# Kernel optimization log

Measured on AMD Instinct MI355X. Metric: run time of the kernel, lower is better.

## Reference

```python
import jax, jax.numpy as jnp
import numpy as np

POWERS = (0, 1, 2)
IN_F, OUT_F = 64, 64
B, N, T = 8, 2048, 12


def setup_inputs() -> dict:
    key = jax.random.key(0)
    ks = jax.random.split(key, 8)
    inp = {
        "x": jax.random.normal(ks[0], (B, IN_F, N, T), dtype=jnp.float32),
        "adj": jax.random.uniform(ks[1], (B, N, N), dtype=jnp.float32),
    }
    # Xavier-uniform weights per adjacency power, zero biases (as in initialize_weights)
    limit = float(np.sqrt(6.0 / (IN_F + OUT_F)))
    for i, p in enumerate(POWERS):
        inp[f"W{p}"] = jax.random.uniform(ks[2 + i], (IN_F, OUT_F), jnp.float32, -limit, limit)
        inp[f"b{p}"] = jnp.zeros((OUT_F,), jnp.float32)
    return inp


def _gcn_conv(x, adj, W, b, a_power):
    # x: [B, F, N, T]; W: [F, O]; adj: [B, N, N]
    h = jnp.einsum('bfnt,fo->bont', x, W) + b[None, :, None, None]
    # repeated diffusion along node axis: h[f, n] <- sum_m adj[n, m] h[f, m]
    for _ in range(a_power):
        h = jnp.einsum('bnm,bomt->bont', adj, h)
    return jax.nn.leaky_relu(h)  # default negative_slope 0.01, same as torch


def reference(x, adj, W0, b0, W1, b1, W2, b2):
    params = {0: (W0, b0), 1: (W1, b1), 2: (W2, b2)}
    outs = [_gcn_conv(x, adj, params[p][0], params[p][1], p) for p in POWERS]
    return jnp.concatenate(outs, axis=1)  # [B, len(POWERS)*O, N, T]
```

## Files before the change

### kernel.cpp

```cpp
#include <hip/hip_runtime.h>

#define B_ 8
#define N_ 2048
#define T_ 12
#define F_ 64
#define NT 24576
#define CH 192
#define C_ 768

typedef __bf16 bf16x8 __attribute__((ext_vector_type(8)));
typedef float f32x4 __attribute__((ext_vector_type(4)));

typedef const __attribute__((address_space(1))) unsigned int as1_uint;
typedef __attribute__((address_space(3))) unsigned int as3_uint;

__device__ __forceinline__ void gload16(const void* g, void* l) {
  __builtin_amdgcn_global_load_lds((as1_uint*)g, (as3_uint*)l, 16, 0, 0);
}

__device__ __forceinline__ unsigned short f2bf(float f) {
  unsigned int u = __float_as_uint(f);
  u += 0x7FFFu + ((u >> 16) & 1u);
  return (unsigned short)(u >> 16);
}

__device__ __forceinline__ float leaky(float v) {
  return v >= 0.0f ? v : 0.01f * v;
}

__global__ __launch_bounds__(256) void convert_adj_k(const float* __restrict__ adj,
                                                     unsigned short* __restrict__ adjb) {
  size_t i = (size_t)blockIdx.x * 256 + threadIdx.x;
  const float4 v = reinterpret_cast<const float4*>(adj)[i];
  ushort4 u;
  u.x = f2bf(v.x); u.y = f2bf(v.y); u.z = f2bf(v.z); u.w = f2bf(v.w);
  reinterpret_cast<ushort4*>(adjb)[i] = u;
}

__device__ __forceinline__ void stage_wt(const float* __restrict__ W,
                                         unsigned short* Wt, int tid) {
  const int f = tid >> 2;
  const int q = tid & 3;
  const float4* row = reinterpret_cast<const float4*>(W + f * 64 + q * 16);
#pragma unroll
  for (int v4 = 0; v4 < 4; ++v4) {
    float4 v = row[v4];
    const int ob = q * 16 + v4 * 4;
    Wt[(ob + 0) * 72 + f] = f2bf(v.x);
    Wt[(ob + 1) * 72 + f] = f2bf(v.y);
    Wt[(ob + 2) * 72 + f] = f2bf(v.z);
    Wt[(ob + 3) * 72 + f] = f2bf(v.w);
  }
}

__global__ __launch_bounds__(256) void p0_k(const float* __restrict__ x,
                                            const float* __restrict__ W0,
                                            const float* __restrict__ bia0,
                                            float* __restrict__ out) {
  __shared__ unsigned short Wt[64 * 72];
  __shared__ float bias[64];
  const int tid = threadIdx.x;
  stage_wt(W0, Wt, tid);
  if (tid < 64) bias[tid] = bia0[tid];
  __syncthreads();

  const int lane = tid & 63;
  const int wave = tid >> 6;
  const int b = blockIdx.y;
  const int e = blockIdx.x * 64 + wave * 16 + (lane & 15);
  const int fgrp = (lane >> 4) * 8;
  const float* xb = x + (size_t)b * F_ * NT;

  bf16x8 xf[2];
#pragma unroll
  for (int kf = 0; kf < 2; ++kf)
#pragma unroll
    for (int j = 0; j < 8; ++j)
      xf[kf][j] = (__bf16)xb[(size_t)(fgrp + kf * 32 + j) * NT + e];

  float* outb = out + (size_t)b * CH * NT;
#pragma unroll
  for (int ob = 0; ob < 4; ++ob) {
    f32x4 acc = {};
#pragma unroll
    for (int kf = 0; kf < 2; ++kf) {
      bf16x8 af = *reinterpret_cast<const bf16x8*>(
          &Wt[(ob * 16 + (lane & 15)) * 72 + kf * 32 + fgrp]);
      acc = __builtin_amdgcn_mfma_f32_16x16x32_bf16(af, xf[kf], acc, 0, 0, 0);
    }
#pragma unroll
    for (int r = 0; r < 4; ++r) {
      const int o = ob * 16 + (lane >> 4) * 4 + r;
      outb[(size_t)o * NT + e] = leaky(acc[r] + bias[o]);
    }
  }
}

__global__ __launch_bounds__(256) void p12_k(const float* __restrict__ x,
                                             const float* __restrict__ W1,
                                             const float* __restrict__ bia1,
                                             const float* __restrict__ W2,
                                             const float* __restrict__ bia2,
                                             unsigned short* __restrict__ G1,
                                             unsigned short* __restrict__ G2) {
  __shared__ unsigned short Wt[2][64 * 72];
  __shared__ float bias[2][64];
  const int tid = threadIdx.x;
  stage_wt(W1, Wt[0], tid);
  stage_wt(W2, Wt[1], tid);
  if (tid < 64) bias[0][tid] = bia1[tid];
  else if (tid < 128) bias[1][tid - 64] = bia2[tid - 64];
  __syncthreads();

  const int lane = tid & 63;
  const int wave = tid >> 6;
  const int b = blockIdx.y;
  const int n = blockIdx.x * 16 + (lane & 15);
  const int fgrp = (lane >> 4) * 8;
  const float* xb = x + (size_t)b * F_ * NT;
  unsigned short* Gp[2] = {G1 + (size_t)b * C_ * N_, G2 + (size_t)b * C_ * N_};

#pragma unroll
  for (int it = 0; it < 3; ++it) {
    const int t = wave * 3 + it;
    const int e = n * T_ + t;

    bf16x8 xf[2];
#pragma unroll
    for (int kf = 0; kf < 2; ++kf)
#pragma unroll
      for (int j = 0; j < 8; ++j)
        xf[kf][j] = (__bf16)xb[(size_t)(fgrp + kf * 32 + j) * NT + e];

#pragma unroll
    for (int p = 0; p < 2; ++p) {
#pragma unroll
      for (int ob = 0; ob < 4; ++ob) {
        f32x4 acc = {};
#pragma unroll
        for (int kf = 0; kf < 2; ++kf) {
          bf16x8 af = *reinterpret_cast<const bf16x8*>(
              &Wt[p][(ob * 16 + (lane & 15)) * 72 + kf * 32 + fgrp]);
          acc = __builtin_amdgcn_mfma_f32_16x16x32_bf16(af, xf[kf], acc, 0, 0, 0);
        }
#pragma unroll
        for (int r = 0; r < 4; ++r) {
          const int o = ob * 16 + (lane >> 4) * 4 + r;
          Gp[p][(size_t)(o * T_ + t) * N_ + n] = f2bf(acc[r] + bias[p][o]);
        }
      }
    }
  }
}

__global__ __launch_bounds__(512, 2) void gemm8_k(
    const unsigned short* __restrict__ adjb,
    const unsigned short* __restrict__ Bt,
    float* __restrict__ out,
    unsigned short* __restrict__ Ht,
    const int mode, const int ochan_base)
{
  extern __shared__ __align__(16) unsigned short lds[];

  const int tid  = threadIdx.x;
  const int lane = tid & 63;
  const int wave = tid >> 6;
  const int wr = wave >> 2;
  const int wc = wave & 3;

  const int b     = blockIdx.x & 7;
  const int w     = blockIdx.x >> 3;
  const int n0    = (w & 7) * 256;
  const int c0    = (w >> 3) * 256;

  const unsigned short* A  = adjb + (size_t)b * N_ * N_;
  const unsigned short* Bm = Bt   + (size_t)b * C_ * N_;

  const unsigned short* aSt = A  + (size_t)(n0 + wave * 32 + (lane >> 2)) * N_ + (lane & 3) * 8;
  const unsigned short* bSt = Bm + (size_t)(c0 + wave * 32 + (lane >> 2)) * N_ + (lane & 3) * 8;
  const int ldsStW = wave * 1024;

  const int aRd = (wr * 128 + (lane & 15)) * 32 + (lane >> 4) * 8;
  const int bRd = (wc * 64  + (lane & 15)) * 32 + (lane >> 4) * 8;

  f32x4 acc[8][4] = {};
  bf16x8 afr[4], bfr[4];

#define STG(BASEG, LDSB, KT, KH) \
  gload16((BASEG) + (KT) * 64 + (KH) * 32, lds + (LDSB) + (KH) * 8192 + ldsStW); \
  gload16((BASEG) + (size_t)16 * N_ + (KT) * 64 + (KH) * 32, \
          lds + (LDSB) + (KH) * 8192 + ldsStW + 512);

#define RD_B(BUFB, KH) { \
  _Pragma("unroll") \
  for (int nf = 0; nf < 4; ++nf) \
    bfr[nf] = *(const bf16x8*)(lds + (BUFB) + (KH) * 8192 + nf * 512 + bRd); }

#define RD_A(BUFA, KH, QM) { \
  _Pragma("unroll") \
  for (int mm = 0; mm < 4; ++mm) \
    afr[mm] = *(const bf16x8*)(lds + (BUFA) + (KH) * 8192 + (QM) * 2048 + mm * 512 + aRd); }

#define MFMA16(QM) { \
  _Pragma("unroll") \
  for (int mm = 0; mm < 4; ++mm) \
  _Pragma("unroll") \
  for (int nf = 0; nf < 4; ++nf) \
    acc[(QM) * 4 + mm][nf] = __builtin_amdgcn_mfma_f32_16x16x32_bf16( \
        afr[mm], bfr[nf], acc[(QM) * 4 + mm][nf], 0, 0, 0); }

#define MIDBAR() \
  __builtin_amdgcn_s_barrier(); \
  asm volatile("s_waitcnt lgkmcnt(0)" ::: "memory"); \
  __builtin_amdgcn_sched_barrier(0); \
  __builtin_amdgcn_s_setprio(1);

#define ENDBAR() \
  __builtin_amdgcn_s_setprio(0); \
  __builtin_amdgcn_s_barrier();

#define WAITV(N) asm volatile("s_waitcnt vmcnt(" #N ")" ::: "memory");

  STG(aSt, 0,     0, 0)  STG(bSt, 32768, 0, 0)
  STG(aSt, 0,     0, 1)  STG(bSt, 32768, 0, 1)
  STG(aSt, 16384, 1, 0)  STG(bSt, 49152, 1, 0)
  WAITV(8)
  __builtin_amdgcn_s_barrier();

#pragma unroll 1
  for (int it = 0; it < 15; ++it) {
    const int kt0 = 2 * it;
    RD_B(32768, 0) RD_A(0, 0, 0)
    STG(aSt, 16384, kt0 + 1, 1)
    MIDBAR() MFMA16(0) ENDBAR()
    RD_A(0, 0, 1)
    STG(bSt, 49152, kt0 + 1, 1)
    WAITV(8)
    MIDBAR() MFMA16(1) ENDBAR()
    RD_B(32768, 1) RD_A(0, 1, 0)
    STG(aSt, 0, kt0 + 2, 0)
    MIDBAR() MFMA16(0) ENDBAR()
    RD_A(0, 1, 1)
    STG(bSt, 32768, kt0 + 2, 0)
    WAITV(8)
    MIDBAR() MFMA16(1) ENDBAR()
    RD_B(49152, 0) RD_A(16384, 0, 0)
    STG(aSt, 0, kt0 + 2, 1)
    MIDBAR() MFMA16(0) ENDBAR()
    RD_A(16384, 0, 1)
    STG(bSt, 32768, kt0 + 2, 1)
    WAITV(8)
    MIDBAR() MFMA16(1) ENDBAR()
    RD_B(49152, 1) RD_A(16384, 1, 0)
    STG(aSt, 16384, kt0 + 3, 0)
    MIDBAR() MFMA16(0) ENDBAR()
    RD_A(16384, 1, 1)
    STG(bSt, 49152, kt0 + 3, 0)
    WAITV(8)
    MIDBAR() MFMA16(1) ENDBAR()
  }

  {
    RD_B(32768, 0) RD_A(0, 0, 0)
    STG(aSt, 16384, 31, 1)
    MIDBAR() MFMA16(0) ENDBAR()
    RD_A(0, 0, 1)
    STG(bSt, 49152, 31, 1)
    WAITV(8)
    MIDBAR() MFMA16(1) ENDBAR()
    RD_B(32768, 1) RD_A(0, 1, 0)
    MIDBAR() MFMA16(0) ENDBAR()
    RD_A(0, 1, 1)
    WAITV(4)
    MIDBAR() MFMA16(1) ENDBAR()
    RD_B(49152, 0) RD_A(16384, 0, 0)
    MIDBAR() MFMA16(0) ENDBAR()
    RD_A(16384, 0, 1)
    WAITV(0)
    MIDBAR() MFMA16(1) ENDBAR()
    RD_B(49152, 1) RD_A(16384, 1, 0)
    MIDBAR() MFMA16(0) ENDBAR()
    RD_A(16384, 1, 1)
    MIDBAR() MFMA16(1) ENDBAR()
  }

  const int r4 = (lane >> 4) * 4;
  if (mode == 0) {
    float* outb = out + (size_t)b * CH * NT;
#pragma unroll
    for (int m = 0; m < 8; ++m) {
#pragma unroll
      for (int nf = 0; nf < 4; ++nf) {
        const int c = c0 + wc * 64 + nf * 16 + (lane & 15);
        const int o = c / 12;
        const int t = c - o * 12;
#pragma unroll
        for (int r = 0; r < 4; ++r) {
          const int n = n0 + wr * 128 + m * 16 + r4 + r;
          outb[((size_t)(ochan_base + o) * N_ + n) * T_ + t] = leaky(acc[m][nf][r]);
        }
      }
    }
  } else {
    unsigned short* Hb = Ht + (size_t)b * C_ * N_;
#pragma unroll
    for (int m = 0; m < 8; ++m) {
#pragma unroll
      for (int nf = 0; nf < 4; ++nf) {
        const int c = c0 + wc * 64 + nf * 16 + (lane & 15);
        const int nb = n0 + wr * 128 + m * 16 + r4;
        ushort4 u;
        u.x = f2bf(acc[m][nf][0]);
        u.y = f2bf(acc[m][nf][1]);
        u.z = f2bf(acc[m][nf][2]);
        u.w = f2bf(acc[m][nf][3]);
        *reinterpret_cast<ushort4*>(&Hb[(size_t)c * N_ + nb]) = u;
      }
    }
  }
#undef STG
#undef RD_B
#undef RD_A
#undef MFMA16
#undef MIDBAR
#undef ENDBAR
#undef WAITV
}

extern "C" void kernel_launch(void* const* d_in, const int* in_sizes, int n_in,
                              void* d_out, int out_size, void* d_ws, size_t ws_size,
                              hipStream_t stream) {
  const float* x   = (const float*)d_in[0];
  const float* adj = (const float*)d_in[1];
  const float* W0  = (const float*)d_in[2];
  const float* b0  = (const float*)d_in[3];
  const float* W1  = (const float*)d_in[4];
  const float* b1  = (const float*)d_in[5];
  const float* W2  = (const float*)d_in[6];
  const float* b2  = (const float*)d_in[7];
  float* out = (float*)d_out;

  char* ws = (char*)d_ws;
  unsigned short* adjb = (unsigned short*)ws;
  unsigned short* G1   = (unsigned short*)(ws + 67108864);
  unsigned short* G2   = (unsigned short*)(ws + 92274688);
  unsigned short* Ht   = G1;

  hipFuncSetAttribute((const void*)gemm8_k,
                      hipFuncAttributeMaxDynamicSharedMemorySize, 131072);

  hipLaunchKernelGGL(convert_adj_k, dim3((B_ * N_ * N_ / 4) / 256), dim3(256), 0, stream,
                     adj, adjb);

  hipLaunchKernelGGL(p0_k, dim3(NT / 64, B_), dim3(256), 0, stream,
                     x, W0, b0, out);

  hipLaunchKernelGGL(p12_k, dim3(N_ / 16, B_), dim3(256), 0, stream,
                     x, W1, b1, W2, b2, G1, G2);

  hipLaunchKernelGGL(gemm8_k, dim3(192), dim3(512), 131072, stream,
                     adjb, G1, out, (unsigned short*)nullptr, 0, 64);

  hipLaunchKernelGGL(gemm8_k, dim3(192), dim3(512), 131072, stream,
                     adjb, G2, out, Ht, 1, 0);

  hipLaunchKernelGGL(gemm8_k, dim3(192), dim3(512), 131072, stream,
                     adjb, Ht, out, (unsigned short*)nullptr, 0, 128);
}
```

Measured before the change: 293.4 us.

## Shrink GEMM column tile to 192 for 256 blocks and swizzle LDS layout

```diff
diff --git a/kernel.cpp b/kernel.cpp
--- a/kernel.cpp
+++ b/kernel.cpp
@@ -168,32 +168,36 @@
   const int wr = wave >> 2;
   const int wc = wave & 3;
 
-  const int b     = blockIdx.x & 7;
-  const int w     = blockIdx.x >> 3;
-  const int n0    = (w & 7) * 256;
-  const int c0    = (w >> 3) * 256;
+  const int b  = blockIdx.x & 7;
+  const int w  = blockIdx.x >> 3;
+  const int n0 = (w & 7) * 256;
+  const int c0 = (w >> 3) * 192;
 
   const unsigned short* A  = adjb + (size_t)b * N_ * N_;
   const unsigned short* Bm = Bt   + (size_t)b * C_ * N_;
 
-  const unsigned short* aSt = A  + (size_t)(n0 + wave * 32 + (lane >> 2)) * N_ + (lane & 3) * 8;
-  const unsigned short* bSt = Bm + (size_t)(c0 + wave * 32 + (lane >> 2)) * N_ + (lane & 3) * 8;
-  const int ldsStW = wave * 1024;
-
-  const int aRd = (wr * 128 + (lane & 15)) * 32 + (lane >> 4) * 8;
-  const int bRd = (wc * 64  + (lane & 15)) * 32 + (lane >> 4) * 8;
-
-  f32x4 acc[8][4] = {};
-  bf16x8 afr[4], bfr[4];
-
-#define STG(BASEG, LDSB, KT, KH) \
-  gload16((BASEG) + (KT) * 64 + (KH) * 32, lds + (LDSB) + (KH) * 8192 + ldsStW); \
-  gload16((BASEG) + (size_t)16 * N_ + (KT) * 64 + (KH) * 32, \
-          lds + (LDSB) + (KH) * 8192 + ldsStW + 512);
+  const int swzSrc = ((lane & 3) ^ ((lane >> 3) & 3)) * 8;
+  const unsigned short* aSt1 = A + (size_t)(n0 + wave * 16 + (lane >> 2)) * N_ + swzSrc;
+  const unsigned short* aSt2 = aSt1 + (size_t)128 * N_;
+  const unsigned short* bSt1 = Bm + (size_t)(c0 + wave * 16 + (lane >> 2)) * N_ + swzSrc;
+  const int brow2 = c0 + 128 + wave * 16 + (lane >> 2);
+  const unsigned short* bSt2 = Bm + (size_t)(brow2 < C_ ? brow2 : C_ - 1) * N_ + swzSrc;
+  const int ldsW = wave * 512;
+
+  const int kg  = (lane >> 4) ^ ((lane >> 1) & 3);
+  const int aRd = (wr * 128 + (lane & 15)) * 32 + kg * 8;
+  const int bRd = (wc * 48  + (lane & 15)) * 32 + kg * 8;
+
+  f32x4 acc[8][3] = {};
+  bf16x8 afr[4], bfr[3];
+
+#define STG(S1, S2, LDSB, KT, KH) \
+  gload16((S1) + (KT) * 64 + (KH) * 32, lds + (LDSB) + (KH) * 8192 + ldsW); \
+  gload16((S2) + (KT) * 64 + (KH) * 32, lds + (LDSB) + (KH) * 8192 + ldsW + 4096);
 
 #define RD_B(BUFB, KH) { \
   _Pragma("unroll") \
-  for (int nf = 0; nf < 4; ++nf) \
+  for (int nf = 0; nf < 3; ++nf) \
     bfr[nf] = *(const bf16x8*)(lds + (BUFB) + (KH) * 8192 + nf * 512 + bRd); }
 
 #define RD_A(BUFA, KH, QM) { \
@@ -201,11 +205,11 @@
   for (int mm = 0; mm < 4; ++mm) \
     afr[mm] = *(const bf16x8*)(lds + (BUFA) + (KH) * 8192 + (QM) * 2048 + mm * 512 + aRd); }
 
-#define MFMA16(QM) { \
+#define MFMA12(QM) { \
   _Pragma("unroll") \
   for (int mm = 0; mm < 4; ++mm) \
   _Pragma("unroll") \
-  for (int nf = 0; nf < 4; ++nf) \
+  for (int nf = 0; nf < 3; ++nf) \
     acc[(QM) * 4 + mm][nf] = __builtin_amdgcn_mfma_f32_16x16x32_bf16( \
         afr[mm], bfr[nf], acc[(QM) * 4 + mm][nf], 0, 0, 0); }
 
@@ -221,9 +225,9 @@
 
 #define WAITV(N) asm volatile("s_waitcnt vmcnt(" #N ")" ::: "memory");
 
-  STG(aSt, 0,     0, 0)  STG(bSt, 32768, 0, 0)
-  STG(aSt, 0,     0, 1)  STG(bSt, 32768, 0, 1)
-  STG(aSt, 16384, 1, 0)  STG(bSt, 49152, 1, 0)
+  STG(aSt1, aSt2, 0,     0, 0)  STG(bSt1, bSt2, 32768, 0, 0)
+  STG(aSt1, aSt2, 0,     0, 1)  STG(bSt1, bSt2, 32768, 0, 1)
+  STG(aSt1, aSt2, 16384, 1, 0)  STG(bSt1, bSt2, 49152, 1, 0)
   WAITV(8)
   __builtin_amdgcn_s_barrier();
 
@@ -231,57 +235,57 @@
   for (int it = 0; it < 15; ++it) {
     const int kt0 = 2 * it;
     RD_B(32768, 0) RD_A(0, 0, 0)
-    STG(aSt, 16384, kt0 + 1, 1)
-    MIDBAR() MFMA16(0) ENDBAR()
+    STG(aSt1, aSt2, 16384, kt0 + 1, 1)
+    MIDBAR() MFMA12(0) ENDBAR()
     RD_A(0, 0, 1)
-    STG(bSt, 49152, kt0 + 1, 1)
-    WAITV(8)
-    MIDBAR() MFMA16(1) ENDBAR()
+    STG(bSt1, bSt2, 49152, kt0 + 1, 1)
+    WAITV(8)
+    MIDBAR() MFMA12(1) ENDBAR()
     RD_B(32768, 1) RD_A(0, 1, 0)
-    STG(aSt, 0, kt0 + 2, 0)
-    MIDBAR() MFMA16(0) ENDBAR()
+    STG(aSt1, aSt2, 0, kt0 + 2, 0)
+    MIDBAR() MFMA12(0) ENDBAR()
     RD_A(0, 1, 1)
-    STG(bSt, 32768, kt0 + 2, 0)
-    WAITV(8)
-    MIDBAR() MFMA16(1) ENDBAR()
+    STG(bSt1, bSt2, 32768, kt0 + 2, 0)
+    WAITV(8)
+    MIDBAR() MFMA12(1) ENDBAR()
     RD_B(49152, 0) RD_A(16384, 0, 0)
-    STG(aSt, 0, kt0 + 2, 1)
-    MIDBAR() MFMA16(0) ENDBAR()
+    STG(aSt1, aSt2, 0, kt0 + 2, 1)
+    MIDBAR() MFMA12(0) ENDBAR()
     RD_A(16384, 0, 1)
-    STG(bSt, 32768, kt0 + 2, 1)
-    WAITV(8)
-    MIDBAR() MFMA16(1) ENDBAR()
+    STG(bSt1, bSt2, 32768, kt0 + 2, 1)
+    WAITV(8)
+    MIDBAR() MFMA12(1) ENDBAR()
     RD_B(49152, 1) RD_A(16384, 1, 0)
-    STG(aSt, 16384, kt0 + 3, 0)
-    MIDBAR() MFMA16(0) ENDBAR()
+    STG(aSt1, aSt2, 16384, kt0 + 3, 0)
+    MIDBAR() MFMA12(0) ENDBAR()
     RD_A(16384, 1, 1)
-    STG(bSt, 49152, kt0 + 3, 0)
-    WAITV(8)
-    MIDBAR() MFMA16(1) ENDBAR()
+    STG(bSt1, bSt2, 49152, kt0 + 3, 0)
+    WAITV(8)
+    MIDBAR() MFMA12(1) ENDBAR()
   }
 
   {
     RD_B(32768, 0) RD_A(0, 0, 0)
-    STG(aSt, 16384, 31, 1)
-    MIDBAR() MFMA16(0) ENDBAR()
+    STG(aSt1, aSt2, 16384, 31, 1)
+    MIDBAR() MFMA12(0) ENDBAR()
     RD_A(0, 0, 1)
-    STG(bSt, 49152, 31, 1)
-    WAITV(8)
-    MIDBAR() MFMA16(1) ENDBAR()
+    STG(bSt1, bSt2, 49152, 31, 1)
+    WAITV(8)
+    MIDBAR() MFMA12(1) ENDBAR()
     RD_B(32768, 1) RD_A(0, 1, 0)
-    MIDBAR() MFMA16(0) ENDBAR()
+    MIDBAR() MFMA12(0) ENDBAR()
     RD_A(0, 1, 1)
     WAITV(4)
-    MIDBAR() MFMA16(1) ENDBAR()
+    MIDBAR() MFMA12(1) ENDBAR()
     RD_B(49152, 0) RD_A(16384, 0, 0)
-    MIDBAR() MFMA16(0) ENDBAR()
+    MIDBAR() MFMA12(0) ENDBAR()
     RD_A(16384, 0, 1)
     WAITV(0)
-    MIDBAR() MFMA16(1) ENDBAR()
+    MIDBAR() MFMA12(1) ENDBAR()
     RD_B(49152, 1) RD_A(16384, 1, 0)
-    MIDBAR() MFMA16(0) ENDBAR()
+    MIDBAR() MFMA12(0) ENDBAR()
     RD_A(16384, 1, 1)
-    MIDBAR() MFMA16(1) ENDBAR()
+    MIDBAR() MFMA12(1) ENDBAR()
   }
 
   const int r4 = (lane >> 4) * 4;
@@ -290,8 +294,8 @@
 #pragma unroll
     for (int m = 0; m < 8; ++m) {
 #pragma unroll
-      for (int nf = 0; nf < 4; ++nf) {
-        const int c = c0 + wc * 64 + nf * 16 + (lane & 15);
+      for (int nf = 0; nf < 3; ++nf) {
+        const int c = c0 + wc * 48 + nf * 16 + (lane & 15);
         const int o = c / 12;
         const int t = c - o * 12;
 #pragma unroll
@@ -306,8 +310,8 @@
 #pragma unroll
     for (int m = 0; m < 8; ++m) {
 #pragma unroll
-      for (int nf = 0; nf < 4; ++nf) {
-        const int c = c0 + wc * 64 + nf * 16 + (lane & 15);
+      for (int nf = 0; nf < 3; ++nf) {
+        const int c = c0 + wc * 48 + nf * 16 + (lane & 15);
         const int nb = n0 + wr * 128 + m * 16 + r4;
         ushort4 u;
         u.x = f2bf(acc[m][nf][0]);
@@ -321,7 +325,7 @@
 #undef STG
 #undef RD_B
 #undef RD_A
-#undef MFMA16
+#undef MFMA12
 #undef MIDBAR
 #undef ENDBAR
 #undef WAITV
@@ -358,12 +362,12 @@
   hipLaunchKernelGGL(p12_k, dim3(N_ / 16, B_), dim3(256), 0, stream,
                      x, W1, b1, W2, b2, G1, G2);
 
-  hipLaunchKernelGGL(gemm8_k, dim3(192), dim3(512), 131072, stream,
+  hipLaunchKernelGGL(gemm8_k, dim3(256), dim3(512), 131072, stream,
                      adjb, G1, out, (unsigned short*)nullptr, 0, 64);
 
-  hipLaunchKernelGGL(gemm8_k, dim3(192), dim3(512), 131072, stream,
+  hipLaunchKernelGGL(gemm8_k, dim3(256), dim3(512), 131072, stream,
                      adjb, G2, out, Ht, 1, 0);
 
-  hipLaunchKernelGGL(gemm8_k, dim3(192), dim3(512), 131072, stream,
+  hipLaunchKernelGGL(gemm8_k, dim3(256), dim3(512), 131072, stream,
                      adjb, Ht, out, (unsigned short*)nullptr, 0, 128);
 }
```

After: 272.4 us. 1.08x faster.
